# Performance work log

Hardware: AMD Instinct MI355X
Metric: run time of the kernel (lower is better)

The kernel has to match this reference:

```python
import jax, jax.numpy as jnp
import numpy as np

CHANNEL = 512
INTER = CHANNEL // 2


def setup_inputs() -> dict:
    key = jax.random.key(0)
    k0, k1, k2, k3, k4 = jax.random.split(key, 5)
    b, c, h, w = 8, CHANNEL, 64, 64
    x = jax.random.normal(k0, (b, c, h, w), dtype=jnp.float32)
    # 1x1 conv weights, no bias: (out_ch, in_ch)
    s_in = 1.0 / np.sqrt(c)
    s_inter = 1.0 / np.sqrt(INTER)
    w_phi = jax.random.uniform(k1, (INTER, c), jnp.float32, -s_in, s_in)
    w_theta = jax.random.uniform(k2, (INTER, c), jnp.float32, -s_in, s_in)
    w_g = jax.random.uniform(k3, (INTER, c), jnp.float32, -s_in, s_in)
    w_mask = jax.random.uniform(k4, (c, INTER), jnp.float32, -s_inter, s_inter)
    return {"x": x, "w_phi": w_phi, "w_theta": w_theta, "w_g": w_g, "w_mask": w_mask}


def reference(x, w_phi, w_theta, w_g, w_mask):
    b, c, h, w = x.shape
    inter = c // 2
    # NOTE: original torch code views the (b, inter, h, w) conv outputs as
    # (b, c, -1), so n = h*w // 2 and the matmul 'feature' dim is the full c.
    n = (h * w) // 2
    phi = jnp.einsum('oc,bchw->bohw', w_phi, x).reshape(b, c, n)        # (b, c, n)
    theta = jnp.einsum('oc,bchw->bohw', w_theta, x).reshape(b, c, n)
    theta = jnp.transpose(theta, (0, 2, 1))                              # (b, n, c)
    g = jnp.einsum('oc,bchw->bohw', w_g, x).reshape(b, c, n)
    g = jnp.transpose(g, (0, 2, 1))                                      # (b, n, c)
    attn = jnp.matmul(theta, phi)                                        # (b, n, n)
    attn = jax.nn.softmax(attn, axis=1)                                  # softmax over dim=1 (columns)
    y = jnp.matmul(attn, g)                                              # (b, n, c)
    y = jnp.transpose(y, (0, 2, 1)).reshape(b, inter, h, w)              # (b, inter, h, w)
    mask = jnp.einsum('oc,bchw->bohw', w_mask, y)                        # (b, c, h, w)
    return mask + x
```

## Files before the change

kernel.cpp:

```cpp
#include <hip/hip_runtime.h>
#include <cstdint>
#include <cstddef>

typedef __attribute__((ext_vector_type(8))) _Float16 half8;
typedef __attribute__((ext_vector_type(8))) short short8;
typedef __attribute__((ext_vector_type(4))) float floatx4;

static __device__ __forceinline__ uint16_t f2h(float f) {
    _Float16 h = (_Float16)f;
    uint16_t u;
    __builtin_memcpy(&u, &h, 2);
    return u;
}
static __device__ __forceinline__ float h2f(uint16_t u) {
    _Float16 h;
    __builtin_memcpy(&h, &u, 2);
    return (float)h;
}
static __device__ __forceinline__ uint16_t f2bf(float f) {
    uint32_t u;
    __builtin_memcpy(&u, &f, 4);
    u += 0x7fffu + ((u >> 16) & 1u);
    return (uint16_t)(u >> 16);
}

static __device__ __forceinline__ void g2lds16(const void* g, void* l) {
    __builtin_amdgcn_global_load_lds((__attribute__((address_space(1))) void*)g,
                                     (__attribute__((address_space(3))) void*)l, 16, 0, 0);
}

__global__ void cvt_weights(const float* __restrict__ wphi, const float* __restrict__ wtheta,
                            const float* __restrict__ wg, const float* __restrict__ wmask,
                            uint16_t* __restrict__ W3, uint16_t* __restrict__ Wm, float* __restrict__ L) {
    int seg = blockIdx.y;
    int i = blockIdx.x * 256 + threadIdx.x;
    if (seg == 4) {
        if (i < 16384) L[i] = 0.f;
        return;
    }
    const float* src = seg == 0 ? wphi : seg == 1 ? wtheta : seg == 2 ? wg : wmask;
    uint16_t* dst = seg < 3 ? W3 + seg * 131072 : Wm;
    int base = i * 4;
    float4 v = *(const float4*)(src + base);
    *(ushort4*)(dst + base) = make_ushort4(f2h(v.x), f2h(v.y), f2h(v.z), f2h(v.w));
}

__global__ __launch_bounds__(256) void transpose_x(const float* __restrict__ x, uint16_t* __restrict__ xt) {
    __shared__ uint16_t tile[64][66];
    int b = blockIdx.z, p0 = blockIdx.x * 64, c0 = blockIdx.y * 64;
    int t0 = threadIdx.x & 63, t1 = threadIdx.x >> 6;
    const float* xb = x + ((long)b * 512 + c0) * 4096 + p0;
#pragma unroll
    for (int r = 0; r < 16; ++r) {
        int cc = t1 * 16 + r;
        tile[cc][t0] = f2h(xb[(long)cc * 4096 + t0]);
    }
    __syncthreads();
    uint16_t* xtb = xt + ((long)b * 4096 + p0) * 512 + c0;
#pragma unroll
    for (int r = 0; r < 16; ++r) {
        int pp = t1 * 16 + r;
        xtb[(long)pp * 512 + t0] = tile[t0][pp];
    }
}

__global__ void scale_g(uint16_t* __restrict__ gc, const float* __restrict__ L) {
    long t = (long)blockIdx.x * 256 + threadIdx.x;
    long base = t * 8;
    int j0 = (int)(base & 2047);
    int b = (int)(base >> 20);
    const float* Lp = L + (long)b * 2048 + j0;
    float4 l0 = *(const float4*)Lp;
    float4 l1 = *(const float4*)(Lp + 4);
    float rr[8] = {1.f / l0.x, 1.f / l0.y, 1.f / l0.z, 1.f / l0.w, 1.f / l1.x, 1.f / l1.y, 1.f / l1.z, 1.f / l1.w};
    uint4 v = *(uint4*)(gc + base);
    uint32_t* pv = (uint32_t*)&v;
    uint32_t o[4];
#pragma unroll
    for (int e = 0; e < 4; ++e) {
        float a = h2f((uint16_t)(pv[e] & 0xffffu)) * rr[2 * e];
        float c = h2f((uint16_t)(pv[e] >> 16)) * rr[2 * e + 1];
        o[e] = (uint32_t)f2bf(a) | ((uint32_t)f2bf(c) << 16);
    }
    *(uint4*)(gc + base) = *(uint4*)o;
}

template <bool KHALF, int EPI, bool SWAP, bool BGATHER, int DT>
__global__ __launch_bounds__(256) void gemm_nt(const uint16_t* __restrict__ A, const uint16_t* __restrict__ B,
                                               void* __restrict__ Cout, const float* __restrict__ resid,
                                               int lda, int ldb, int ldc, int nK,
                                               long aBatch, long bBatch, long cBatch,
                                               void* __restrict__ Cout2, int ldc2, long c2Batch,
                                               float* __restrict__ Lsum) {
    __shared__ uint16_t Al[2 * 128 * 32];
    __shared__ uint16_t Bl[2 * 128 * 32];
    const int b = blockIdx.z;
    const uint16_t* Ab = A + (long)b * aBatch;
    const uint16_t* Bb = B + (long)b * bBatch;
    const int m0 = (SWAP ? blockIdx.y : blockIdx.x) * 128;
    const int n0 = (SWAP ? blockIdx.x : blockIdx.y) * 128;
    const int tid = threadIdx.x;
    const int lane = tid & 63, wave = tid >> 6;
    const int ln = lane & 15, q = lane >> 4;
    const int wm = (wave & 1) * 64, wn = (wave >> 1) * 64;

    floatx4 acc[4][4];
#pragma unroll
    for (int i = 0; i < 4; ++i)
#pragma unroll
        for (int j = 0; j < 4; ++j) acc[i][j] = (floatx4){0.f, 0.f, 0.f, 0.f};

    for (int kt = 0; kt < nK; ++kt) {
        int k0 = kt * 64;
#pragma unroll
        for (int half = 0; half < 2; ++half) {
            int kh = k0 + half * 32;
            int keff = kh;
            long roff = 0;
            if (KHALF && kh >= 256) { keff = kh - 256; roff = 2048; }
            uint16_t* AlH = &Al[half * 4096];
            uint16_t* BlH = &Bl[half * 4096];
#pragma unroll
            for (int s = 0; s < 2; ++s) {
                int c = tid + s * 256;
                int row = c >> 2, kq = (c & 3) * 8;
                g2lds16(Ab + ((long)(m0 + row) + roff) * lda + keff + kq, &AlH[c * 8]);
                if (BGATHER) {
                    int pg = n0 + row;
                    int ii = pg & 2047, hh = pg >> 11;
                    const uint16_t* src = Bb + (long)ii * 512 + 2 * (keff + kq);
                    uint4 v0 = *(const uint4*)src;
                    uint4 v1 = *(const uint4*)(src + 8);
                    uint32_t* a = (uint32_t*)&v0;
                    uint32_t* cc = (uint32_t*)&v1;
                    uint32_t o[4];
                    if (hh == 0) {
                        o[0] = (a[0] & 0xffffu) | (a[1] << 16);
                        o[1] = (a[2] & 0xffffu) | (a[3] << 16);
                        o[2] = (cc[0] & 0xffffu) | (cc[1] << 16);
                        o[3] = (cc[2] & 0xffffu) | (cc[3] << 16);
                    } else {
                        o[0] = (a[0] >> 16) | (a[1] & 0xffff0000u);
                        o[1] = (a[2] >> 16) | (a[3] & 0xffff0000u);
                        o[2] = (cc[0] >> 16) | (cc[1] & 0xffff0000u);
                        o[3] = (cc[2] >> 16) | (cc[3] & 0xffff0000u);
                    }
                    *(uint4*)&BlH[c * 8] = *(uint4*)o;
                } else {
                    g2lds16(Bb + ((long)(n0 + row) + roff) * ldb + keff + kq, &BlH[c * 8]);
                }
            }
        }
        __syncthreads();
#pragma unroll
        for (int half = 0; half < 2; ++half) {
            const uint16_t* AlH = &Al[half * 4096];
            const uint16_t* BlH = &Bl[half * 4096];
            short8 af[4], bfr[4];
#pragma unroll
            for (int mt = 0; mt < 4; ++mt) af[mt] = *(const short8*)&AlH[(wm + mt * 16 + ln) * 32 + q * 8];
#pragma unroll
            for (int nt = 0; nt < 4; ++nt) bfr[nt] = *(const short8*)&BlH[(wn + nt * 16 + ln) * 32 + q * 8];
#pragma unroll
            for (int mt = 0; mt < 4; ++mt)
#pragma unroll
                for (int nt = 0; nt < 4; ++nt) {
                    if constexpr (DT == 0) {
                        half8 ah, bh;
                        __builtin_memcpy(&ah, &af[mt], 16);
                        __builtin_memcpy(&bh, &bfr[nt], 16);
                        acc[mt][nt] = __builtin_amdgcn_mfma_f32_16x16x32_f16(ah, bh, acc[mt][nt], 0, 0, 0);
                    } else {
                        acc[mt][nt] = __builtin_amdgcn_mfma_f32_16x16x32_bf16(af[mt], bfr[nt], acc[mt][nt], 0, 0, 0);
                    }
                }
        }
        __syncthreads();
    }

    if (EPI == 0 || (EPI == 3 && n0 < 512)) {
        uint16_t* C = (uint16_t*)Cout + (long)b * cBatch;
#pragma unroll
        for (int mt = 0; mt < 4; ++mt)
#pragma unroll
            for (int r = 0; r < 4; ++r) {
                int gm = m0 + wm + mt * 16 + q * 4 + r;
#pragma unroll
                for (int nt = 0; nt < 4; ++nt) {
                    int gn = n0 + wn + nt * 16 + ln;
                    C[(long)gm * ldc + gn] = f2h(acc[mt][nt][r]);
                }
            }
    } else if (EPI == 4) {
        uint16_t* C = (uint16_t*)Cout + (long)b * cBatch;
        float cs[4] = {0.f, 0.f, 0.f, 0.f};
#pragma unroll
        for (int mt = 0; mt < 4; ++mt)
#pragma unroll
            for (int r = 0; r < 4; ++r) {
                int gm = m0 + wm + mt * 16 + q * 4 + r;
#pragma unroll
                for (int nt = 0; nt < 4; ++nt) {
                    int gn = n0 + wn + nt * 16 + ln;
                    float e = __expf(acc[mt][nt][r] - 12.f);
                    C[(long)gm * ldc + gn] = f2bf(e);
                    cs[nt] += e;
                }
            }
#pragma unroll
        for (int nt = 0; nt < 4; ++nt) {
            float s = cs[nt];
            s += __shfl_xor(s, 16);
            s += __shfl_xor(s, 32);
            if (q == 0) atomicAdd(&Lsum[(long)b * 2048 + n0 + wn + nt * 16 + ln], s);
        }
    } else if (EPI == 1) {
        float* C = (float*)Cout + (long)b * cBatch;
        const float* X = resid + (long)b * cBatch;
#pragma unroll
        for (int mt = 0; mt < 4; ++mt)
#pragma unroll
            for (int r = 0; r < 4; ++r) {
                int gm = m0 + wm + mt * 16 + q * 4 + r;
#pragma unroll
                for (int nt = 0; nt < 4; ++nt) {
                    int gn = n0 + wn + nt * 16 + ln;
                    long idx = (long)gm * ldc + gn;
                    C[idx] = acc[mt][nt][r] + X[idx];
                }
            }
    } else {
        uint16_t* C = (uint16_t*)Cout2 + (long)b * c2Batch;
#pragma unroll
        for (int nt = 0; nt < 4; ++nt) {
            int gn2 = n0 - 512 + wn + nt * 16 + ln;
#pragma unroll
            for (int mt = 0; mt < 4; ++mt) {
                int gmB = m0 + wm + mt * 16 + q * 4;
                ushort4 u = make_ushort4(f2h(acc[mt][nt][0]), f2h(acc[mt][nt][1]), f2h(acc[mt][nt][2]),
                                         f2h(acc[mt][nt][3]));
                *(ushort4*)&C[(long)gn2 * ldc2 + gmB] = u;
            }
        }
    }
}

extern "C" void kernel_launch(void* const* d_in, const int* in_sizes, int n_in, void* d_out, int out_size, void* d_ws,
                              size_t ws_size, hipStream_t stream) {
    const float* x = (const float*)d_in[0];
    const float* wphi = (const float*)d_in[1];
    const float* wtheta = (const float*)d_in[2];
    const float* wg = (const float*)d_in[3];
    const float* wmask = (const float*)d_in[4];
    float* out = (float*)d_out;
    char* ws = (char*)d_ws;

    uint16_t* W3 = (uint16_t*)(ws + 0);
    uint16_t* Wm = (uint16_t*)(ws + 786432);
    float* L = (float*)(ws + 1048576);
    char* A_region = ws + 1179648;
    char* B_region = ws + 68288512;
    uint16_t* Xt = (uint16_t*)A_region;
    uint16_t* P = (uint16_t*)A_region;
    uint16_t* C2 = (uint16_t*)B_region;
    uint16_t* Y2 = (uint16_t*)B_region;
    uint16_t* Gc = (uint16_t*)(B_region + 33554432);

    cvt_weights<<<dim3(128, 5), 256, 0, stream>>>(wphi, wtheta, wg, wmask, W3, Wm, L);

    transpose_x<<<dim3(64, 8, 8), 256, 0, stream>>>(x, Xt);

    gemm_nt<false, 3, false, false, 0><<<dim3(32, 6, 8), 256, 0, stream>>>(
        Xt, W3, C2, nullptr, 512, 512, 512, 8, 4096L * 512, 0, 4096L * 512, Gc, 4096, 256L * 4096, nullptr);

    gemm_nt<true, 4, false, false, 0><<<dim3(16, 16, 8), 256, 0, stream>>>(
        C2 + 256, C2, P, nullptr, 512, 512, 2048, 8, 4096L * 512, 4096L * 512, 2048L * 2048, nullptr, 0, 0, L);

    scale_g<<<4096, 256, 0, stream>>>(Gc, L);

    gemm_nt<false, 0, true, false, 1><<<dim3(4, 16, 8), 256, 0, stream>>>(
        P, Gc, Y2, nullptr, 2048, 2048, 512, 32, 2048L * 2048, 1048576L, 2048L * 512, nullptr, 0, 0, nullptr);

    gemm_nt<false, 1, false, true, 0><<<dim3(4, 32, 8), 256, 0, stream>>>(
        Wm, Y2, out, x, 256, 512, 4096, 4, 0, 1048576L, 512L * 4096, nullptr, 0, 0, nullptr);
}
```

Baseline: 295.6 us.

## Permute tile columns consistently so the exp and G epilogues write vectorized stores

The exp epilogue now writes each lane's four values as one 8-byte store instead of four scattered 2-byte stores. To make that possible it applies a fixed column permutation within each 64-wide tile of P and of the softmax sums. The G-producing epilogue applies the same permutation to its rows, so the P·G reduction stays correct. The constant -12 offset is folded into the accumulator's initial value, and the first GEMM's grid is swapped to change block ordering. This relies on both permutations staying in sync across kernels.

```diff
diff --git a/kernel.cpp b/kernel.cpp
--- a/kernel.cpp
+++ b/kernel.cpp
@@ -85,7 +85,7 @@
     *(uint4*)(gc + base) = *(uint4*)o;
 }
 
-template <bool KHALF, int EPI, bool SWAP, bool BGATHER, int DT>
+template <bool KHALF, int EPI, bool SWAP, int BMODE, int DT>
 __global__ __launch_bounds__(256) void gemm_nt(const uint16_t* __restrict__ A, const uint16_t* __restrict__ B,
                                                void* __restrict__ Cout, const float* __restrict__ resid,
                                                int lda, int ldb, int ldc, int nK,
@@ -104,11 +104,12 @@
     const int ln = lane & 15, q = lane >> 4;
     const int wm = (wave & 1) * 64, wn = (wave >> 1) * 64;
 
+    const float ainit = (EPI == 4) ? -12.f : 0.f;
     floatx4 acc[4][4];
 #pragma unroll
     for (int i = 0; i < 4; ++i)
 #pragma unroll
-        for (int j = 0; j < 4; ++j) acc[i][j] = (floatx4){0.f, 0.f, 0.f, 0.f};
+        for (int j = 0; j < 4; ++j) acc[i][j] = (floatx4){ainit, ainit, ainit, ainit};
 
     for (int kt = 0; kt < nK; ++kt) {
         int k0 = kt * 64;
@@ -125,7 +126,9 @@
                 int c = tid + s * 256;
                 int row = c >> 2, kq = (c & 3) * 8;
                 g2lds16(Ab + ((long)(m0 + row) + roff) * lda + keff + kq, &AlH[c * 8]);
-                if (BGATHER) {
+                if (BMODE == 0) {
+                    g2lds16(Bb + ((long)(n0 + row) + roff) * ldb + keff + kq, &BlH[c * 8]);
+                } else {
                     int pg = n0 + row;
                     int ii = pg & 2047, hh = pg >> 11;
                     const uint16_t* src = Bb + (long)ii * 512 + 2 * (keff + kq);
@@ -146,8 +149,6 @@
                         o[3] = (cc[2] >> 16) | (cc[3] & 0xffff0000u);
                     }
                     *(uint4*)&BlH[c * 8] = *(uint4*)o;
-                } else {
-                    g2lds16(Bb + ((long)(n0 + row) + roff) * ldb + keff + kq, &BlH[c * 8]);
                 }
             }
         }
@@ -193,26 +194,29 @@
             }
     } else if (EPI == 4) {
         uint16_t* C = (uint16_t*)Cout + (long)b * cBatch;
+        const int cb = n0 + wn + (ln << 2);
         float cs[4] = {0.f, 0.f, 0.f, 0.f};
 #pragma unroll
         for (int mt = 0; mt < 4; ++mt)
 #pragma unroll
             for (int r = 0; r < 4; ++r) {
                 int gm = m0 + wm + mt * 16 + q * 4 + r;
-#pragma unroll
-                for (int nt = 0; nt < 4; ++nt) {
-                    int gn = n0 + wn + nt * 16 + ln;
-                    float e = __expf(acc[mt][nt][r] - 12.f);
-                    C[(long)gm * ldc + gn] = f2bf(e);
-                    cs[nt] += e;
-                }
+                float e0 = __expf(acc[mt][0][r]);
+                float e1 = __expf(acc[mt][1][r]);
+                float e2 = __expf(acc[mt][2][r]);
+                float e3 = __expf(acc[mt][3][r]);
+                cs[0] += e0; cs[1] += e1; cs[2] += e2; cs[3] += e3;
+                uint2 wv;
+                wv.x = (uint32_t)f2bf(e0) | ((uint32_t)f2bf(e1) << 16);
+                wv.y = (uint32_t)f2bf(e2) | ((uint32_t)f2bf(e3) << 16);
+                *(uint2*)&C[(long)gm * ldc + cb] = wv;
             }
 #pragma unroll
         for (int nt = 0; nt < 4; ++nt) {
             float s = cs[nt];
             s += __shfl_xor(s, 16);
             s += __shfl_xor(s, 32);
-            if (q == 0) atomicAdd(&Lsum[(long)b * 2048 + n0 + wn + nt * 16 + ln], s);
+            if (q == 0) atomicAdd(&Lsum[(long)b * 2048 + cb + nt], s);
         }
     } else if (EPI == 1) {
         float* C = (float*)Cout + (long)b * cBatch;
@@ -231,15 +235,16 @@
             }
     } else {
         uint16_t* C = (uint16_t*)Cout2 + (long)b * c2Batch;
+        const int cb = m0 + wm + q * 16;
 #pragma unroll
         for (int nt = 0; nt < 4; ++nt) {
             int gn2 = n0 - 512 + wn + nt * 16 + ln;
-#pragma unroll
-            for (int mt = 0; mt < 4; ++mt) {
-                int gmB = m0 + wm + mt * 16 + q * 4;
-                ushort4 u = make_ushort4(f2h(acc[mt][nt][0]), f2h(acc[mt][nt][1]), f2h(acc[mt][nt][2]),
-                                         f2h(acc[mt][nt][3]));
-                *(ushort4*)&C[(long)gn2 * ldc2 + gmB] = u;
+            uint16_t* rowp = C + (long)gn2 * ldc2 + cb;
+#pragma unroll
+            for (int r = 0; r < 4; ++r) {
+                ushort4 u = make_ushort4(f2h(acc[0][nt][r]), f2h(acc[1][nt][r]),
+                                         f2h(acc[2][nt][r]), f2h(acc[3][nt][r]));
+                *(ushort4*)&rowp[r * 4] = u;
             }
         }
     }
@@ -270,17 +275,17 @@
 
     transpose_x<<<dim3(64, 8, 8), 256, 0, stream>>>(x, Xt);
 
-    gemm_nt<false, 3, false, false, 0><<<dim3(32, 6, 8), 256, 0, stream>>>(
+    gemm_nt<false, 3, true, 0, 0><<<dim3(6, 32, 8), 256, 0, stream>>>(
         Xt, W3, C2, nullptr, 512, 512, 512, 8, 4096L * 512, 0, 4096L * 512, Gc, 4096, 256L * 4096, nullptr);
 
-    gemm_nt<true, 4, false, false, 0><<<dim3(16, 16, 8), 256, 0, stream>>>(
+    gemm_nt<true, 4, false, 0, 0><<<dim3(16, 16, 8), 256, 0, stream>>>(
         C2 + 256, C2, P, nullptr, 512, 512, 2048, 8, 4096L * 512, 4096L * 512, 2048L * 2048, nullptr, 0, 0, L);
 
     scale_g<<<4096, 256, 0, stream>>>(Gc, L);
 
-    gemm_nt<false, 0, true, false, 1><<<dim3(4, 16, 8), 256, 0, stream>>>(
+    gemm_nt<false, 0, true, 0, 1><<<dim3(4, 16, 8), 256, 0, stream>>>(
         P, Gc, Y2, nullptr, 2048, 2048, 512, 32, 2048L * 2048, 1048576L, 2048L * 512, nullptr, 0, 0, nullptr);
 
-    gemm_nt<false, 1, false, true, 0><<<dim3(4, 32, 8), 256, 0, stream>>>(
+    gemm_nt<false, 1, false, 1, 0><<<dim3(4, 32, 8), 256, 0, stream>>>(
         Wm, Y2, out, x, 256, 512, 4096, 4, 0, 1048576L, 512L * 4096, nullptr, 0, 0, nullptr);
 }
```

Result: slower. 317.3 us (+7.3%).
